# Optimization experiments

Hardware: AMD Instinct MI355X
Metric: run time of the kernel (lower is better)

## Reference

```python
import jax, jax.numpy as jnp
import numpy as np

EPS = 1e-6
DIM, HEADS, HEAD_DIM, FFN = 1024, 16, 64, 4096
B, S = 2, 2048


def layer_norm(x, g, b):
    m = jnp.mean(x, axis=-1, keepdims=True)
    v = jnp.mean(jnp.square(x - m), axis=-1, keepdims=True)
    return (x - m) * jax.lax.rsqrt(v + EPS) * g + b


def apply_rope(x, cos, sin):
    # x: (b, h, s, d); cos/sin: (s, d) broadcast over b, h
    x1, x2 = jnp.split(x, 2, axis=-1)
    rot = jnp.concatenate([-x2, x1], axis=-1)
    return x * cos + rot * sin


def setup_inputs() -> dict:
    key = jax.random.key(0)
    ks = jax.random.split(key, 24)
    sc_in = 1.0 / np.sqrt(DIM)
    sc_ffn = 1.0 / np.sqrt(FFN)
    inp = {
        "x": jax.random.normal(ks[0], (B, S, DIM), jnp.float32),
        "rope_cos": jax.random.uniform(ks[1], (S, HEAD_DIM), jnp.float32),
        "rope_sin": jax.random.uniform(ks[2], (S, HEAD_DIM), jnp.float32),
        "w_qkv": jax.random.normal(ks[3], (3 * DIM, DIM), jnp.float32) * sc_in,
        "b_qkv": jnp.zeros((3 * DIM,), jnp.float32),
        "w_out": jax.random.normal(ks[4], (DIM, DIM), jnp.float32) * sc_in,
        "b_out": jnp.zeros((DIM,), jnp.float32),
        "qn_g": jnp.ones((DIM,), jnp.float32),
        "qn_b": jnp.zeros((DIM,), jnp.float32),
        "kn_g": jnp.ones((DIM,), jnp.float32),
        "kn_b": jnp.zeros((DIM,), jnp.float32),
        "ln1_g": jnp.ones((DIM,), jnp.float32),
        "ln1_b": jnp.zeros((DIM,), jnp.float32),
        "ln2_g": jnp.ones((DIM,), jnp.float32),
        "ln2_b": jnp.zeros((DIM,), jnp.float32),
        "w1": jax.random.normal(ks[5], (FFN, DIM), jnp.float32) * sc_in,
        "b1": jnp.zeros((FFN,), jnp.float32),
        "w2": jax.random.normal(ks[6], (DIM, FFN), jnp.float32) * sc_ffn,
        "b2": jnp.zeros((DIM,), jnp.float32),
        "w3": jax.random.normal(ks[7], (FFN, DIM), jnp.float32) * sc_in,
        "b3": jnp.zeros((FFN,), jnp.float32),
    }
    return inp


def reference(x, rope_cos, rope_sin, w_qkv, b_qkv, w_out, b_out,
              qn_g, qn_b, kn_g, kn_b, ln1_g, ln1_b, ln2_g, ln2_b,
              w1, b1, w2, b2, w3, b3):
    bs, s, d = x.shape
    # --- pre-norm self-attention ---
    h = layer_norm(x, ln1_g, ln1_b)
    qkv = h @ w_qkv.T + b_qkv                      # (b, s, 3d)
    q, k, v = jnp.split(qkv, 3, axis=-1)
    q = layer_norm(q, qn_g, qn_b)                  # QK-norm over full dim
    k = layer_norm(k, kn_g, kn_b)
    # (b, s, d) -> (b, h, s, hd)
    q = q.reshape(bs, s, HEADS, HEAD_DIM).transpose(0, 2, 1, 3)
    k = k.reshape(bs, s, HEADS, HEAD_DIM).transpose(0, 2, 1, 3)
    v = v.reshape(bs, s, HEADS, HEAD_DIM).transpose(0, 2, 1, 3)
    q = apply_rope(q, rope_cos, rope_sin)
    k = apply_rope(k, rope_cos, rope_sin)
    scale = 1.0 / np.sqrt(HEAD_DIM)
    scores = jnp.einsum('bhqd,bhkd->bhqk', q, k) * scale
    probs = jax.nn.softmax(scores, axis=-1)
    attn = jnp.einsum('bhqk,bhkd->bhqd', probs, v)
    attn = attn.transpose(0, 2, 1, 3).reshape(bs, s, d)
    x = x + (attn @ w_out.T + b_out)
    # --- pre-norm SwiGLU FFN ---
    h2 = layer_norm(x, ln2_g, ln2_b)
    ffn = (jax.nn.silu(h2 @ w1.T + b1) * (h2 @ w3.T + b3)) @ w2.T + b2
    return x + ffn
```

## Files before the change

kernel.cpp:

```cpp
#include <hip/hip_runtime.h>
#include <hip/hip_bf16.h>


typedef __bf16 bf16_t;
typedef bf16_t bf16x8 __attribute__((ext_vector_type(8)));
typedef bf16_t bf16x4 __attribute__((ext_vector_type(4)));
typedef float  f32x4  __attribute__((ext_vector_type(4)));
typedef float  f32x16 __attribute__((ext_vector_type(16)));

#define DIM   1024
#define HEADS 16
#define HD    64
#define FFND  4096
#define NB    2
#define SEQ   2048
#define NTOK  (NB * SEQ)

#define GLOAD16(gp, lp) __builtin_amdgcn_global_load_lds( \
    (const __attribute__((address_space(1))) void*)(gp),  \
    (__attribute__((address_space(3))) void*)(lp), 16, 0, 0)

#define CVTPK(lo, hi_) ({ unsigned r_;                                        \
  asm("v_cvt_pk_bf16_f32 %0, %1, %2" : "=v"(r_) : "v"(lo), "v"(hi_)); r_; })
#define PLSWAP(a, b) asm("v_permlane32_swap_b32 %0, %1" : "+v"(a), "+v"(b))
#define SBAR() asm volatile("s_barrier" ::: "memory")

#define F2B_S0 786432
#define F2B_S1 262144
#define F2B_S2 1048576
#define F2B_S3 1048576
#define F2B_S4 1048576
#define F2B_C1 (F2B_S0)
#define F2B_C2 (F2B_C1 + F2B_S1)
#define F2B_C3 (F2B_C2 + F2B_S2)
#define F2B_C4 (F2B_C3 + F2B_S3)
#define F2B_N  (F2B_C4 + F2B_S4)

__global__ void f2bf_all_kernel(const float* __restrict__ s0, const float* __restrict__ s1,
                                const float* __restrict__ s2, const float* __restrict__ s3,
                                const float* __restrict__ s4,
                                bf16_t* __restrict__ d0, bf16_t* __restrict__ d1,
                                bf16_t* __restrict__ d2, bf16_t* __restrict__ d3,
                                bf16_t* __restrict__ d4) {
  int idx = blockIdx.x * blockDim.x + threadIdx.x;
  int stride = gridDim.x * blockDim.x;
  for (; idx < F2B_N; idx += stride) {
    const float* src; bf16_t* dst; int i;
    if (idx < F2B_C1)      { src = s0; dst = d0; i = idx; }
    else if (idx < F2B_C2) { src = s1; dst = d1; i = idx - F2B_C1; }
    else if (idx < F2B_C3) { src = s2; dst = d2; i = idx - F2B_C2; }
    else if (idx < F2B_C4) { src = s3; dst = d3; i = idx - F2B_C3; }
    else                   { src = s4; dst = d4; i = idx - F2B_C4; }
    float4 v = reinterpret_cast<const float4*>(src)[i];
    bf16x4 o;
    o[0] = (bf16_t)v.x; o[1] = (bf16_t)v.y; o[2] = (bf16_t)v.z; o[3] = (bf16_t)v.w;
    reinterpret_cast<bf16x4*>(dst)[i] = o;
  }
}

__global__ __launch_bounds__(256) void ln_kernel(
    const float* __restrict__ x, const float* __restrict__ g,
    const float* __restrict__ b, bf16_t* __restrict__ out) {
  int t = blockIdx.x;
  int i = threadIdx.x;
  float4 v = reinterpret_cast<const float4*>(x + (size_t)t * DIM)[i];
  float s  = v.x + v.y + v.z + v.w;
  float s2 = v.x * v.x + v.y * v.y + v.z * v.z + v.w * v.w;
#pragma unroll
  for (int off = 32; off > 0; off >>= 1) {
    s  += __shfl_down(s, off, 64);
    s2 += __shfl_down(s2, off, 64);
  }
  __shared__ float red[2][4];
  int wid = i >> 6, lane = i & 63;
  if (lane == 0) { red[0][wid] = s; red[1][wid] = s2; }
  __syncthreads();
  float S  = red[0][0] + red[0][1] + red[0][2] + red[0][3];
  float S2 = red[1][0] + red[1][1] + red[1][2] + red[1][3];
  float mean = S * (1.0f / DIM);
  float var  = S2 * (1.0f / DIM) - mean * mean;
  float r = rsqrtf(var + 1e-6f);
  float vv[4] = {v.x, v.y, v.z, v.w};
  bf16x4 o;
#pragma unroll
  for (int j = 0; j < 4; ++j) {
    int d = i * 4 + j;
    o[j] = (bf16_t)((vv[j] - mean) * r * g[d] + b[d]);
  }
  *reinterpret_cast<bf16x4*>(out + (size_t)t * DIM + i * 4) = o;
}

template <int OUT_MODE>
__global__ __launch_bounds__(512, 2) void gemm256(
    const bf16_t* __restrict__ A, const bf16_t* __restrict__ B,
    const float* __restrict__ bias, const bf16_t* __restrict__ comp,
    void* __restrict__ Cout, int M, int N, int Kfull, int Klen) {
  __shared__ __align__(16) bf16_t Al[2][256][64];
  __shared__ __align__(16) bf16_t Bl[2][256][64];
  const int nTn = N >> 8;
  const int nwg = gridDim.x;
  const int bid = blockIdx.x;
  const int swz = ((nwg & 7) == 0) ? ((bid & 7) * (nwg >> 3) + (bid >> 3)) : bid;
  const int bm = swz / nTn, bn = swz % nTn;
  const int k0base = blockIdx.z * Klen;
  const int NT = Klen >> 6;
  const int tid = threadIdx.x, wid = tid >> 6, lane = tid & 63;
  const int wm2 = wid >> 2, wn = wid & 3;
  const int lr = lane & 15, lg = lane >> 4;
  const int strow = wid * 8 + (lane >> 3);
  const int stg   = ((lane & 7) ^ ((lane >> 3) & 7)) << 3;
  const bf16_t* Abase = A + (size_t)(bm * 256 + strow) * Kfull + k0base + stg;
  const bf16_t* Bbase = B + (size_t)(bn * 256 + strow) * Kfull + k0base + stg;

#define STAGE_A(buf, half, c, t)                                              \
  GLOAD16(Abase + (size_t)((half) * 128 + (c) * 64) * Kfull + (t) * 64,       \
          &Al[buf][(half) * 128 + (c) * 64 + wid * 8][0])
#define STAGE_B(buf, half, c, t)                                              \
  GLOAD16(Bbase + (size_t)((half) * 128 + (c) * 64) * Kfull + (t) * 64,       \
          &Bl[buf][(half) * 128 + (c) * 64 + wid * 8][0])

  f32x4 acc[8][4] = {};
  STAGE_A(0, 0, 0, 0); STAGE_A(0, 0, 1, 0); STAGE_A(0, 1, 0, 0); STAGE_A(0, 1, 1, 0);
  STAGE_B(0, 0, 0, 0); STAGE_B(0, 0, 1, 0); STAGE_B(0, 1, 0, 0); STAGE_B(0, 1, 1, 0);

  for (int t = 0; t < NT; ++t) {
    const int cur = t & 1, nxt = cur ^ 1;
    asm volatile("s_waitcnt vmcnt(0)" ::: "memory");
    SBAR();
    if (t + 1 < NT) {
      STAGE_A(nxt, 0, 0, t + 1); STAGE_A(nxt, 0, 1, t + 1);
      STAGE_A(nxt, 1, 0, t + 1); STAGE_A(nxt, 1, 1, t + 1);
      STAGE_B(nxt, 0, 0, t + 1); STAGE_B(nxt, 0, 1, t + 1);
      STAGE_B(nxt, 1, 0, t + 1); STAGE_B(nxt, 1, 1, t + 1);
    }
#pragma unroll
    for (int ks = 0; ks < 2; ++ks) {
      bf16x8 af[8], bfr[4];
#pragma unroll
      for (int nf = 0; nf < 4; ++nf) {
        const int row = wn * 64 + nf * 16 + lr;
        const int g = ((ks * 4 + lg) ^ (lane & 7)) << 3;
        bfr[nf] = *reinterpret_cast<const bf16x8*>(&Bl[cur][row][g]);
      }
#pragma unroll
      for (int mf = 0; mf < 8; ++mf) {
        const int row = wm2 * 128 + mf * 16 + lr;
        const int g = ((ks * 4 + lg) ^ (lane & 7)) << 3;
        af[mf] = *reinterpret_cast<const bf16x8*>(&Al[cur][row][g]);
      }
      __builtin_amdgcn_s_setprio(1);
#pragma unroll
      for (int mf = 0; mf < 8; ++mf)
#pragma unroll
        for (int nf = 0; nf < 4; ++nf)
          acc[mf][nf] = __builtin_amdgcn_mfma_f32_16x16x32_bf16(af[mf], bfr[nf], acc[mf][nf], 0, 0, 0);
      __builtin_amdgcn_s_setprio(0);
    }
  }
#undef STAGE_A
#undef STAGE_B
  const int r0 = lg * 4;
#pragma unroll
  for (int mf = 0; mf < 8; ++mf) {
#pragma unroll
    for (int r = 0; r < 4; ++r) {
      const int row = bm * 256 + wm2 * 128 + mf * 16 + r0 + r;
#pragma unroll
      for (int nf = 0; nf < 4; ++nf) {
        const int col = bn * 256 + wn * 64 + nf * 16 + lr;
        float v = acc[mf][nf][r];
        if (OUT_MODE == 1) {
          v += bias[col];
          reinterpret_cast<bf16_t*>(Cout)[(size_t)row * N + col] = (bf16_t)v;
        } else if (OUT_MODE == 2) {
          float* P = reinterpret_cast<float*>(Cout) + (size_t)blockIdx.z * M * N;
          P[(size_t)row * N + col] = v;
        } else {
          v += bias[col];
          float c1 = (float)comp[(size_t)row * N + col];
          float sg = c1 / (1.0f + __expf(-c1));
          reinterpret_cast<bf16_t*>(Cout)[(size_t)row * N + col] = (bf16_t)(sg * v);
        }
      }
    }
  }
}

__global__ void combine_kernel(const float* __restrict__ part,
                               const float* __restrict__ bias,
                               const float* __restrict__ res,
                               float* __restrict__ out, int n4) {
  const int slice = NTOK * DIM / 4;
  int i = blockIdx.x * blockDim.x + threadIdx.x;
  int stride = gridDim.x * blockDim.x;
  const float4* p = reinterpret_cast<const float4*>(part);
  const float4* r4 = reinterpret_cast<const float4*>(res);
  const float4* b4 = reinterpret_cast<const float4*>(bias);
  float4* o4 = reinterpret_cast<float4*>(out);
  for (; i < n4; i += stride) {
    float4 a = p[i], b = p[i + slice], c = p[i + 2 * slice], d = p[i + 3 * slice];
    float4 rr = r4[i];
    float4 bb = b4[i & 255];
    float4 o;
    o.x = a.x + b.x + c.x + d.x + bb.x + rr.x;
    o.y = a.y + b.y + c.y + d.y + bb.y + rr.y;
    o.z = a.z + b.z + c.z + d.z + bb.z + rr.z;
    o.w = a.w + b.w + c.w + d.w + bb.w + rr.w;
    o4[i] = o;
  }
}

template <int OUT_MODE>
__global__ __launch_bounds__(256) void gemm_bt(
    const bf16_t* __restrict__ A, const bf16_t* __restrict__ B,
    const float* __restrict__ bias, const float* __restrict__ res,
    void* __restrict__ Cout, int M, int N, int Kfull, int Klen) {
  __shared__ bf16_t As[128][32];
  __shared__ bf16_t Bs[128][32];
  const int nTn = N >> 7;
  const int nwg = gridDim.x;
  const int bid = blockIdx.x;
  const int swz = ((nwg & 7) == 0) ? ((bid & 7) * (nwg >> 3) + (bid >> 3)) : bid;
  const int bm = swz / nTn;
  const int bn = swz % nTn;
  const int k0base = blockIdx.z * Klen;
  const int tid  = threadIdx.x;
  const int wid  = tid >> 6;
  const int lane = tid & 63;
  const int wm = (wid >> 1) * 64, wn = (wid & 1) * 64;
  const int lr = lane & 15;
  const int gq = lane >> 4;
  const int sr = lane >> 2;
  const int sg = lane & 3;
  const int cS = ((sg ^ ((sr >> 1) & 3)) << 3);
  const int swg = ((gq ^ ((lr >> 1) & 3)) << 3);
  f32x4 acc[4][4] = {};
  const bf16_t* Ag0 = A + (size_t)(bm * 128 + wid * 16 + sr) * Kfull + k0base + cS;
  const bf16_t* Ag1 = Ag0 + (size_t)64 * Kfull;
  const bf16_t* Bg0 = B + (size_t)(bn * 128 + wid * 16 + sr) * Kfull + k0base + cS;
  const bf16_t* Bg1 = Bg0 + (size_t)64 * Kfull;
  bf16_t* ldsA0 = &As[wid * 16][0];
  bf16_t* ldsA1 = &As[64 + wid * 16][0];
  bf16_t* ldsB0 = &Bs[wid * 16][0];
  bf16_t* ldsB1 = &Bs[64 + wid * 16][0];
  for (int k0 = 0; k0 < Klen; k0 += 32) {
    __syncthreads();
    GLOAD16(Ag0 + k0, ldsA0);
    GLOAD16(Ag1 + k0, ldsA1);
    GLOAD16(Bg0 + k0, ldsB0);
    GLOAD16(Bg1 + k0, ldsB1);
    __syncthreads();
    bf16x8 af[4], bfr[4];
#pragma unroll
    for (int mi = 0; mi < 4; ++mi)
      af[mi] = *reinterpret_cast<const bf16x8*>(&As[wm + mi * 16 + lr][swg]);
#pragma unroll
    for (int ni = 0; ni < 4; ++ni)
      bfr[ni] = *reinterpret_cast<const bf16x8*>(&Bs[wn + ni * 16 + lr][swg]);
#pragma unroll
    for (int mi = 0; mi < 4; ++mi)
#pragma unroll
      for (int ni = 0; ni < 4; ++ni)
        acc[mi][ni] = __builtin_amdgcn_mfma_f32_16x16x32_bf16(af[mi], bfr[ni], acc[mi][ni], 0, 0, 0);
  }
  const int r0 = (lane >> 4) * 4;
#pragma unroll
  for (int mi = 0; mi < 4; ++mi) {
#pragma unroll
    for (int r = 0; r < 4; ++r) {
      int row = bm * 128 + wm + mi * 16 + r0 + r;
#pragma unroll
      for (int ni = 0; ni < 4; ++ni) {
        int col = bn * 128 + wn + ni * 16 + lr;
        float v = acc[mi][ni][r];
        if (OUT_MODE == 0) {
          v += bias[col] + res[(size_t)row * N + col];
          reinterpret_cast<float*>(Cout)[(size_t)row * N + col] = v;
        } else {
          float* P = reinterpret_cast<float*>(Cout) + (size_t)blockIdx.z * M * N;
          P[(size_t)row * N + col] = v;
        }
      }
    }
  }
}

__global__ __launch_bounds__(256) void qknorm_rope_kernel(
    const bf16_t* __restrict__ qkv,
    const float* __restrict__ qg, const float* __restrict__ qb,
    const float* __restrict__ kg, const float* __restrict__ kb,
    const float* __restrict__ rc, const float* __restrict__ rs,
    bf16_t* __restrict__ q_r, bf16_t* __restrict__ k_r) {
  int t = blockIdx.x;
  int b = t >> 11, s = t & 2047;
  const bf16_t* p = qkv + (size_t)t * 3072;
  int i = threadIdx.x;
  bf16x4 qv = *reinterpret_cast<const bf16x4*>(p + i * 4);
  bf16x4 kv = *reinterpret_cast<const bf16x4*>(p + 1024 + i * 4);
  float q4[4], k4[4];
  float sq = 0.f, sq2 = 0.f, sk = 0.f, sk2 = 0.f;
#pragma unroll
  for (int j = 0; j < 4; ++j) {
    q4[j] = (float)qv[j]; k4[j] = (float)kv[j];
    sq += q4[j]; sq2 += q4[j] * q4[j];
    sk += k4[j]; sk2 += k4[j] * k4[j];
  }
#pragma unroll
  for (int off = 32; off > 0; off >>= 1) {
    sq  += __shfl_down(sq, off, 64);
    sq2 += __shfl_down(sq2, off, 64);
    sk  += __shfl_down(sk, off, 64);
    sk2 += __shfl_down(sk2, off, 64);
  }
  __shared__ float red[4][4];
  int wid = i >> 6, lane = i & 63;
  if (lane == 0) { red[0][wid] = sq; red[1][wid] = sq2; red[2][wid] = sk; red[3][wid] = sk2; }
  __syncthreads();
  float Sq  = red[0][0] + red[0][1] + red[0][2] + red[0][3];
  float Sq2 = red[1][0] + red[1][1] + red[1][2] + red[1][3];
  float Sk  = red[2][0] + red[2][1] + red[2][2] + red[2][3];
  float Sk2 = red[3][0] + red[3][1] + red[3][2] + red[3][3];
  float mq = Sq * (1.0f / DIM);
  float vq = Sq2 * (1.0f / DIM) - mq * mq;
  float rq = rsqrtf(vq + 1e-6f);
  float mk = Sk * (1.0f / DIM);
  float vk = Sk2 * (1.0f / DIM) - mk * mk;
  float rk = rsqrtf(vk + 1e-6f);
  const float QS = 0.18033688011f;
  float qn[4], kn[4];
#pragma unroll
  for (int j = 0; j < 4; ++j) {
    int d = i * 4 + j;
    qn[j] = (q4[j] - mq) * rq * qg[d] + qb[d];
    kn[j] = (k4[j] - mk) * rk * kg[d] + kb[d];
  }
#pragma unroll
  for (int j = 0; j < 4; ++j) {
    int d = i * 4 + j, h = d >> 6, hd = d & 63;
    float c  = rc[s * HD + hd];
    float sn = rs[s * HD + hd];
    float qpn = __shfl_xor(qn[j], 8, 64);
    float kpn = __shfl_xor(kn[j], 8, 64);
    float qo = qn[j] * c + ((hd < 32) ? -qpn : qpn) * sn;
    float ko = kn[j] * c + ((hd < 32) ? -kpn : kpn) * sn;
    size_t oi = ((size_t)(b * HEADS + h) * SEQ + s) * HD + hd;
    q_r[oi] = (bf16_t)(qo * QS);
    k_r[oi] = (bf16_t)ko;
  }
}

__global__ __launch_bounds__(256) void vtrans_kernel(
    const bf16_t* __restrict__ qkv, bf16_t* __restrict__ v_t) {
  __shared__ bf16_t T[64][72];
  const int st = blockIdx.x;
  const int bh = blockIdx.y;
  const int b = bh >> 4, h = bh & 15;
  const int tid = threadIdx.x;
  const int r = tid >> 2, c = (tid & 3) * 8;
  const bf16_t* src = qkv + (size_t)(b * SEQ + st * 64 + r) * 3072 + 2048 + h * 64;
  *reinterpret_cast<bf16x8*>(&T[r][c])      = *reinterpret_cast<const bf16x8*>(src + c);
  *reinterpret_cast<bf16x8*>(&T[r][c + 32]) = *reinterpret_cast<const bf16x8*>(src + c + 32);
  __syncthreads();
  bf16x8 o0, o1;
#pragma unroll
  for (int j = 0; j < 8; ++j) { o0[j] = T[c + j][r]; o1[j] = T[c + 32 + j][r]; }
  bf16_t* dst = v_t + ((size_t)bh * 64 + r) * SEQ + st * 64;
  *reinterpret_cast<bf16x8*>(dst + c)      = o0;
  *reinterpret_cast<bf16x8*>(dst + c + 32) = o1;
}

__global__ __launch_bounds__(512, 2) void attn_kernel(
    const bf16_t* __restrict__ q_r, const bf16_t* __restrict__ k_r,
    const bf16_t* __restrict__ v_t, bf16_t* __restrict__ attn_out) {
  __shared__ __align__(16) char smem[69632];
  bf16_t* KsB = (bf16_t*)smem;
  bf16_t* VsB = (bf16_t*)(smem + 32768);
  float*  Xch = (float*)smem;
  const int bid = blockIdx.x;
  const int hh = bid & 31;
  const int qt = bid >> 5;
  const int bidx = hh >> 4, h = hh & 15;
  const int tid = threadIdx.x, wid = tid >> 6, lane = tid & 63;
  const int kh = wid >> 2, ww = wid & 3;
  const int lq = lane & 31, hi = lane >> 5;
  const int qA = qt * 256 + ww * 64 + lq;
  const int qB = qA + 32;
  const bf16_t* Qp = q_r + (size_t)hh * SEQ * HD;
  const bf16_t* Kp = k_r + (size_t)hh * SEQ * HD + (size_t)kh * 1024 * HD;
  const bf16_t* Vp = v_t + (size_t)hh * HD * SEQ + kh * 1024;
  bf16_t* Ks0 = KsB + kh * 2 * 4096;
  bf16_t* Vs0 = VsB + kh * 2 * 4096;
  bf16x8 qfA[4], qfB[4];
#pragma unroll
  for (int kdt = 0; kdt < 4; ++kdt) {
    qfA[kdt] = *reinterpret_cast<const bf16x8*>(Qp + (size_t)qA * HD + kdt * 16 + hi * 8);
    qfB[kdt] = *reinterpret_cast<const bf16x8*>(Qp + (size_t)qB * HD + kdt * 16 + hi * 8);
  }
  f32x16 oA0 = {}, oA1 = {}, oB0 = {}, oB1 = {};
  float lA = 0.f, lB = 0.f;
  const int kSrcA = lane * HD + ww * 8;
  const int kSrcB = lane * HD + (ww + 4) * 8;
  const int vSrcA = lane * SEQ + ww * 8;
  const int vSrcB = lane * SEQ + (ww + 4) * 8;
  const int ldsA = ww * 512;
  const int ldsB = 2048 + ww * 512;
  GLOAD16(Kp + kSrcA, &Ks0[ldsA]);
  GLOAD16(Kp + kSrcB, &Ks0[ldsB]);
  GLOAD16(Vp + vSrcA, &Vs0[ldsA]);
  GLOAD16(Vp + vSrcB, &Vs0[ldsB]);
  __syncthreads();
  const int NT = 1024 / 64;
  for (int kt = 0; kt < NT; ++kt) {
    const int cur = kt & 1, nxt = cur ^ 1;
    if (kt + 1 < NT) {
      GLOAD16(Kp + (kt + 1) * (64 * HD) + kSrcA, &Ks0[nxt * 4096 + ldsA]);
      GLOAD16(Kp + (kt + 1) * (64 * HD) + kSrcB, &Ks0[nxt * 4096 + ldsB]);
      GLOAD16(Vp + (kt + 1) * 64 + vSrcA, &Vs0[nxt * 4096 + ldsA]);
      GLOAD16(Vp + (kt + 1) * 64 + vSrcB, &Vs0[nxt * 4096 + ldsB]);
    }
    f32x16 sA0 = {}, sA1 = {}, sB0 = {}, sB1 = {};
#pragma unroll
    for (int kdt = 0; kdt < 4; ++kdt) {
      const int goff = cur * 4096 + (kdt * 2 + hi) * 512;
      bf16x8 kf0 = *reinterpret_cast<const bf16x8*>(&Ks0[goff + lq * 8]);
      bf16x8 kf1 = *reinterpret_cast<const bf16x8*>(&Ks0[goff + (lq + 32) * 8]);
      sA0 = __builtin_amdgcn_mfma_f32_32x32x16_bf16(kf0, qfA[kdt], sA0, 0, 0, 0);
      sA1 = __builtin_amdgcn_mfma_f32_32x32x16_bf16(kf1, qfA[kdt], sA1, 0, 0, 0);
      sB0 = __builtin_amdgcn_mfma_f32_32x32x16_bf16(kf0, qfB[kdt], sB0, 0, 0, 0);
      sB1 = __builtin_amdgcn_mfma_f32_32x32x16_bf16(kf1, qfB[kdt], sB1, 0, 0, 0);
    }
#pragma unroll
    for (int i = 0; i < 16; ++i) sA0[i] = __builtin_amdgcn_exp2f(sA0[i]);
#pragma unroll
    for (int i = 0; i < 16; ++i) sA1[i] = __builtin_amdgcn_exp2f(sA1[i]);
#pragma unroll
    for (int i = 0; i < 16; ++i) sB0[i] = __builtin_amdgcn_exp2f(sB0[i]);
#pragma unroll
    for (int i = 0; i < 16; ++i) sB1[i] = __builtin_amdgcn_exp2f(sB1[i]);
    {
      f32x16 t = sA0 + sA1;
      float a = ((t[0] + t[8]) + (t[4] + t[12])) + ((t[2] + t[10]) + (t[6] + t[14]));
      float b = ((t[1] + t[9]) + (t[5] + t[13])) + ((t[3] + t[11]) + (t[7] + t[15]));
      lA += a + b;
      f32x16 u = sB0 + sB1;
      float c = ((u[0] + u[8]) + (u[4] + u[12])) + ((u[2] + u[10]) + (u[6] + u[14]));
      float d = ((u[1] + u[9]) + (u[5] + u[13])) + ((u[3] + u[11]) + (u[7] + u[15]));
      lB += c + d;
    }
#pragma unroll
    for (int tt = 0; tt < 2; ++tt) {
#pragma unroll
      for (int ks = 0; ks < 2; ++ks) {
        const f32x16& pA = tt ? sA1 : sA0;
        const f32x16& pB = tt ? sB1 : sB0;
        unsigned a0, b0, c0, d0, a1, b1, c1, d1;
        if (ks == 0) {
          a0 = CVTPK(pA[0], pA[1]); b0 = CVTPK(pA[4], pA[5]);
          c0 = CVTPK(pA[2], pA[3]); d0 = CVTPK(pA[6], pA[7]);
          a1 = CVTPK(pB[0], pB[1]); b1 = CVTPK(pB[4], pB[5]);
          c1 = CVTPK(pB[2], pB[3]); d1 = CVTPK(pB[6], pB[7]);
        } else {
          a0 = CVTPK(pA[8], pA[9]);   b0 = CVTPK(pA[12], pA[13]);
          c0 = CVTPK(pA[10], pA[11]); d0 = CVTPK(pA[14], pA[15]);
          a1 = CVTPK(pB[8], pB[9]);   b1 = CVTPK(pB[12], pB[13]);
          c1 = CVTPK(pB[10], pB[11]); d1 = CVTPK(pB[14], pB[15]);
        }
        PLSWAP(a0, b0); PLSWAP(c0, d0); PLSWAP(a1, b1); PLSWAP(c1, d1);
        union { unsigned u[4]; bf16x8 v; } pfA, pfB;
        pfA.u[0] = a0; pfA.u[1] = c0; pfA.u[2] = b0; pfA.u[3] = d0;
        pfB.u[0] = a1; pfB.u[1] = c1; pfB.u[2] = b1; pfB.u[3] = d1;
        const int gv = cur * 4096 + (tt * 4 + ks * 2 + hi) * 512;
        bf16x8 vf0 = *reinterpret_cast<const bf16x8*>(&Vs0[gv + lq * 8]);
        bf16x8 vf1 = *reinterpret_cast<const bf16x8*>(&Vs0[gv + (lq + 32) * 8]);
        oA0 = __builtin_amdgcn_mfma_f32_32x32x16_bf16(vf0, pfA.v, oA0, 0, 0, 0);
        oA1 = __builtin_amdgcn_mfma_f32_32x32x16_bf16(vf1, pfA.v, oA1, 0, 0, 0);
        oB0 = __builtin_amdgcn_mfma_f32_32x32x16_bf16(vf0, pfB.v, oB0, 0, 0, 0);
        oB1 = __builtin_amdgcn_mfma_f32_32x32x16_bf16(vf1, pfB.v, oB1, 0, 0, 0);
      }
    }
    __syncthreads();
  }
  lA += __shfl_xor(lA, 32, 64);
  lB += __shfl_xor(lB, 32, 64);
  if (kh == 1) {
    float* my = Xch + (size_t)(ww * 64 + lane) * 68;
#pragma unroll
    for (int g = 0; g < 4; ++g) {
      *reinterpret_cast<float4*>(my + g * 4)      = make_float4(oA0[g*4], oA0[g*4+1], oA0[g*4+2], oA0[g*4+3]);
      *reinterpret_cast<float4*>(my + 16 + g * 4) = make_float4(oA1[g*4], oA1[g*4+1], oA1[g*4+2], oA1[g*4+3]);
      *reinterpret_cast<float4*>(my + 32 + g * 4) = make_float4(oB0[g*4], oB0[g*4+1], oB0[g*4+2], oB0[g*4+3]);
      *reinterpret_cast<float4*>(my + 48 + g * 4) = make_float4(oB1[g*4], oB1[g*4+1], oB1[g*4+2], oB1[g*4+3]);
    }
    my[64] = lA; my[65] = lB;
  }
  __syncthreads();
  if (kh == 0) {
    const float* pr = Xch + (size_t)(ww * 64 + lane) * 68;
#pragma unroll
    for (int i = 0; i < 16; ++i) {
      oA0[i] += pr[i];      oA1[i] += pr[16 + i];
      oB0[i] += pr[32 + i]; oB1[i] += pr[48 + i];
    }
    float invA = 1.0f / (lA + pr[64]);
    float invB = 1.0f / (lB + pr[65]);
    bf16_t* orowA = attn_out + ((size_t)(bidx * SEQ + qA)) * DIM + h * 64;
    bf16_t* orowB = attn_out + ((size_t)(bidx * SEQ + qB)) * DIM + h * 64;
#pragma unroll
    for (int g = 0; g < 4; ++g) {
      bf16x4 wA0, wA1, wB0, wB1;
#pragma unroll
      for (int j = 0; j < 4; ++j) {
        wA0[j] = (bf16_t)(oA0[g * 4 + j] * invA);
        wA1[j] = (bf16_t)(oA1[g * 4 + j] * invA);
        wB0[j] = (bf16_t)(oB0[g * 4 + j] * invB);
        wB1[j] = (bf16_t)(oB1[g * 4 + j] * invB);
      }
      *reinterpret_cast<bf16x4*>(orowA + g * 8 + 4 * hi)      = wA0;
      *reinterpret_cast<bf16x4*>(orowA + 32 + g * 8 + 4 * hi) = wA1;
      *reinterpret_cast<bf16x4*>(orowB + g * 8 + 4 * hi)      = wB0;
      *reinterpret_cast<bf16x4*>(orowB + 32 + g * 8 + 4 * hi) = wB1;
    }
  }
}

extern "C" void kernel_launch(void* const* d_in, const int* in_sizes, int n_in,
                              void* d_out, int out_size, void* d_ws, size_t ws_size,
                              hipStream_t stream) {
  const float* x        = (const float*)d_in[0];
  const float* rope_cos = (const float*)d_in[1];
  const float* rope_sin = (const float*)d_in[2];
  const float* w_qkv    = (const float*)d_in[3];
  const float* b_qkv    = (const float*)d_in[4];
  const float* w_out    = (const float*)d_in[5];
  const float* b_out    = (const float*)d_in[6];
  const float* qn_g     = (const float*)d_in[7];
  const float* qn_b     = (const float*)d_in[8];
  const float* kn_g     = (const float*)d_in[9];
  const float* kn_b     = (const float*)d_in[10];
  const float* ln1_g    = (const float*)d_in[11];
  const float* ln1_b    = (const float*)d_in[12];
  const float* ln2_g    = (const float*)d_in[13];
  const float* ln2_b    = (const float*)d_in[14];
  const float* w1       = (const float*)d_in[15];
  const float* b1       = (const float*)d_in[16];
  const float* w2       = (const float*)d_in[17];
  const float* b2       = (const float*)d_in[18];
  const float* w3       = (const float*)d_in[19];
  const float* b3       = (const float*)d_in[20];

  const size_t OFF_WQKV = 0;
  const size_t OFF_WOUT = 6291456;
  const size_t OFF_W1   = 8388608;
  const size_t OFF_W2   = 16777216;
  const size_t OFF_W3   = 25165824;
  const size_t OFF_H1   = 33554432;
  const size_t OFF_QKV  = 41943040;
  const size_t OFF_QR   = 67108864;
  const size_t OFF_KR   = 75497472;
  const size_t OFF_VT   = 83886080;
  const size_t OFF_ATT  = 92274688;
  const size_t OFF_X2   = 100663296;
  const size_t OFF_H2   = 117440512;
  const size_t OFF_PART = 125829120;
  const size_t NEEDED   = 125829120;
  const size_t NEED_SPLIT = OFF_PART + 67108864;
  if (ws_size < NEEDED) return;
  const bool use_split = (ws_size >= NEED_SPLIT);

  char* ws = (char*)d_ws;
  bf16_t* wqkv_bf = (bf16_t*)(ws + OFF_WQKV);
  bf16_t* wout_bf = (bf16_t*)(ws + OFF_WOUT);
  bf16_t* w1_bf   = (bf16_t*)(ws + OFF_W1);
  bf16_t* w2_bf   = (bf16_t*)(ws + OFF_W2);
  bf16_t* w3_bf   = (bf16_t*)(ws + OFF_W3);
  bf16_t* h1      = (bf16_t*)(ws + OFF_H1);
  bf16_t* qkv     = (bf16_t*)(ws + OFF_QKV);
  bf16_t* q_r     = (bf16_t*)(ws + OFF_QR);
  bf16_t* k_r     = (bf16_t*)(ws + OFF_KR);
  bf16_t* v_t     = (bf16_t*)(ws + OFF_VT);
  bf16_t* att     = (bf16_t*)(ws + OFF_ATT);
  float*  x2      = (float*)(ws + OFF_X2);
  bf16_t* h2      = (bf16_t*)(ws + OFF_H2);
  bf16_t* a1      = (bf16_t*)(ws + OFF_H1);
  bf16_t* a3      = (bf16_t*)(ws + OFF_QR);
  float*  part    = (float*)(ws + OFF_PART);
  float*  out     = (float*)d_out;

  f2bf_all_kernel<<<2048, 256, 0, stream>>>(w_qkv, w_out, w1, w2, w3,
                                            wqkv_bf, wout_bf, w1_bf, w2_bf, w3_bf);
  ln_kernel<<<NTOK, 256, 0, stream>>>(x, ln1_g, ln1_b, h1);
  gemm256<1><<<dim3(192, 1, 1), 512, 0, stream>>>(h1, wqkv_bf, b_qkv, nullptr, qkv,
                                                  NTOK, 3072, DIM, DIM);
  qknorm_rope_kernel<<<NTOK, 256, 0, stream>>>(qkv, qn_g, qn_b, kn_g, kn_b,
                                               rope_cos, rope_sin, q_r, k_r);
  vtrans_kernel<<<dim3(SEQ / 64, NB * HEADS), 256, 0, stream>>>(qkv, v_t);
  attn_kernel<<<256, 512, 0, stream>>>(q_r, k_r, v_t, att);
  gemm_bt<0><<<dim3(32 * 8, 1, 1), 256, 0, stream>>>(
      att, wout_bf, b_out, x, x2, NTOK, DIM, DIM, DIM);
  ln_kernel<<<NTOK, 256, 0, stream>>>(x2, ln2_g, ln2_b, h2);
  gemm256<1><<<dim3(256, 1, 1), 512, 0, stream>>>(h2, w1_bf, b1, nullptr, a1,
                                                  NTOK, FFND, DIM, DIM);
  gemm256<3><<<dim3(256, 1, 1), 512, 0, stream>>>(h2, w3_bf, b3, a1, a3,
                                                  NTOK, FFND, DIM, DIM);
  if (use_split) {
    gemm256<2><<<dim3(64, 1, 4), 512, 0, stream>>>(a3, w2_bf, nullptr, nullptr, part,
                                                   NTOK, DIM, FFND, FFND / 4);
    combine_kernel<<<2048, 256, 0, stream>>>(part, b2, x2, out, NTOK * DIM / 4);
  } else {
    gemm_bt<0><<<dim3(32 * 8, 1, 1), 256, 0, stream>>>(
        a3, w2_bf, b2, x2, out, NTOK, DIM, FFND, FFND);
  }
}
```

Before: 286.9 us.

## Interleave split A/B tile prefetch with sub-tiled MFMA phases in GEMM loop

The GEMM main loop now issues the A-tile prefetch before the barrier and waits only on older loads (vmcnt(4)) instead of draining every outstanding load. The 8x4 MFMA block is split into four phases of two M-fragments each, with LDS fragment reads and the B-tile prefetch placed between phases and barriers around each phase. The aim is to overlap global-to-LDS traffic and LDS reads with matrix work and to lower register pressure from holding all A fragments at once. In exchange each K-step now has many more workgroup barriers, which could serialize waves.

```diff
diff --git a/kernel.cpp b/kernel.cpp
--- a/kernel.cpp
+++ b/kernel.cpp
@@ -125,36 +125,67 @@
 
   for (int t = 0; t < NT; ++t) {
     const int cur = t & 1, nxt = cur ^ 1;
-    asm volatile("s_waitcnt vmcnt(0)" ::: "memory");
-    SBAR();
-    if (t + 1 < NT) {
+    const bool pf = (t + 1 < NT);
+    if (pf) {
       STAGE_A(nxt, 0, 0, t + 1); STAGE_A(nxt, 0, 1, t + 1);
       STAGE_A(nxt, 1, 0, t + 1); STAGE_A(nxt, 1, 1, t + 1);
-      STAGE_B(nxt, 0, 0, t + 1); STAGE_B(nxt, 0, 1, t + 1);
-      STAGE_B(nxt, 1, 0, t + 1); STAGE_B(nxt, 1, 1, t + 1);
-    }
-#pragma unroll
-    for (int ks = 0; ks < 2; ++ks) {
-      bf16x8 af[8], bfr[4];
-#pragma unroll
-      for (int nf = 0; nf < 4; ++nf) {
+      asm volatile("s_waitcnt vmcnt(4)" ::: "memory");
+    } else {
+      asm volatile("s_waitcnt vmcnt(0)" ::: "memory");
+    }
+    SBAR();
+    bf16x8 bfr[4][2], af[2][2];
+#pragma unroll
+    for (int nf = 0; nf < 4; ++nf)
+#pragma unroll
+      for (int ks = 0; ks < 2; ++ks) {
         const int row = wn * 64 + nf * 16 + lr;
         const int g = ((ks * 4 + lg) ^ (lane & 7)) << 3;
-        bfr[nf] = *reinterpret_cast<const bf16x8*>(&Bl[cur][row][g]);
+        bfr[nf][ks] = *reinterpret_cast<const bf16x8*>(&Bl[cur][row][g]);
       }
 #pragma unroll
-      for (int mf = 0; mf < 8; ++mf) {
-        const int row = wm2 * 128 + mf * 16 + lr;
+    for (int i = 0; i < 2; ++i)
+#pragma unroll
+      for (int ks = 0; ks < 2; ++ks) {
+        const int row = wm2 * 128 + i * 16 + lr;
         const int g = ((ks * 4 + lg) ^ (lane & 7)) << 3;
-        af[mf] = *reinterpret_cast<const bf16x8*>(&Al[cur][row][g]);
+        af[i][ks] = *reinterpret_cast<const bf16x8*>(&Al[cur][row][g]);
       }
+    __builtin_amdgcn_s_setprio(1);
+#pragma unroll
+    for (int i = 0; i < 2; ++i)
+#pragma unroll
+      for (int nf = 0; nf < 4; ++nf)
+#pragma unroll
+        for (int ks = 0; ks < 2; ++ks)
+          acc[i][nf] = __builtin_amdgcn_mfma_f32_16x16x32_bf16(af[i][ks], bfr[nf][ks], acc[i][nf], 0, 0, 0);
+    __builtin_amdgcn_s_setprio(0);
+    SBAR();
+#pragma unroll
+    for (int p = 1; p < 4; ++p) {
+#pragma unroll
+      for (int i = 0; i < 2; ++i)
+#pragma unroll
+        for (int ks = 0; ks < 2; ++ks) {
+          const int row = wm2 * 128 + (p * 2 + i) * 16 + lr;
+          const int g = ((ks * 4 + lg) ^ (lane & 7)) << 3;
+          af[i][ks] = *reinterpret_cast<const bf16x8*>(&Al[cur][row][g]);
+        }
+      if (p == 1 && pf) {
+        STAGE_B(nxt, 0, 0, t + 1); STAGE_B(nxt, 0, 1, t + 1);
+        STAGE_B(nxt, 1, 0, t + 1); STAGE_B(nxt, 1, 1, t + 1);
+      }
+      SBAR();
       __builtin_amdgcn_s_setprio(1);
 #pragma unroll
-      for (int mf = 0; mf < 8; ++mf)
+      for (int i = 0; i < 2; ++i)
 #pragma unroll
         for (int nf = 0; nf < 4; ++nf)
-          acc[mf][nf] = __builtin_amdgcn_mfma_f32_16x16x32_bf16(af[mf], bfr[nf], acc[mf][nf], 0, 0, 0);
+#pragma unroll
+          for (int ks = 0; ks < 2; ++ks)
+            acc[p * 2 + i][nf] = __builtin_amdgcn_mfma_f32_16x16x32_bf16(af[i][ks], bfr[nf][ks], acc[p * 2 + i][nf], 0, 0, 0);
       __builtin_amdgcn_s_setprio(0);
+      SBAR();
     }
   }
 #undef STAGE_A
```

After: 307.1 us. 7.0% more time.
